# Kernel tuning notes

Measured on AMD Instinct MI355X. Metric: run time of the kernel, lower is better.

Reference implementation:

```python
import jax, jax.numpy as jnp
import numpy as np

ARITY = 4  # matches init_kwargs; params.shape[1] == 2**ARITY


def _high_order_act(X, params):
    # X: [B, G*arity], params: [G, 2**arity, O]
    B = X.shape[0]
    G, _, O = params.shape
    a = ARITY
    A = X.reshape(B, G, a)
    # sort ascending along the arity dim (torch.sort returns values + indices)
    A_ind = jnp.argsort(A, axis=2)                      # [B, G, a] int32
    A_sort = jnp.take_along_axis(A, A_ind, axis=2)      # [B, G, a]
    # barycentric-style coefficients: smallest value, then successive diffs
    coef = jnp.concatenate(
        [A_sort[:, :, :1], A_sort[:, :, 1:] - A_sort[:, :, :-1]], axis=2
    )                                                   # [B, G, a]
    # bit-power index: reverse cumsum of 2**A_ind -> suffix sums of bit masks
    pow2 = jnp.left_shift(jnp.int32(1), A_ind.astype(jnp.int32))  # [B, G, a]
    idx = jnp.cumsum(pow2[:, :, ::-1], axis=2)[:, :, ::-1]        # [B, G, a], in [1, 2**a - 1]
    # gather per-group table rows: params[g, idx[b,g,k], :]
    g_idx = jnp.arange(G)[None, :, None]                # [1, G, 1]
    gathered = params[g_idx, idx]                       # [B, G, a, O]
    # einsum 'jikl,ijk->ijl' in torch (j=G, i=B) == 'bgao,bga->bgo' here
    out = jnp.einsum('bgao,bga->bgo', gathered, coef)   # [B, G, O]
    return out.reshape(B, G * O)


def setup_inputs() -> dict:
    key = jax.random.key(0)
    kx, kp = jax.random.split(key)
    B, G, a, O = 8192, 256, ARITY, 16
    X = jax.random.normal(kx, (B, G * a), dtype=jnp.float32)
    params = jax.random.normal(kp, (G, 2 ** a, O), dtype=jnp.float32)
    return {"X": X, "params": params}


def reference(X, params):
    return _high_order_act(X, params)
```

## Files before the change

### kernel.cpp

```cpp
#include <hip/hip_runtime.h>


typedef float f32x4 __attribute__((ext_vector_type(4)));

#define NT 512
#define TG 16
#define ROWS 64
#define RPW 8
#define TSTRIDE 260

__global__ __launch_bounds__(NT, 4) void hoa_kernel(
    const float* __restrict__ X, const float* __restrict__ P,
    float* __restrict__ out, int B, int G)
{
    __shared__ float lds[TG * TSTRIDE];

    const int tid = threadIdx.x;
    const int g0 = blockIdx.x * TG;
    const int b0 = blockIdx.y * ROWS;

#pragma unroll
    for (int i = 0; i < 2; ++i) {
        int idx = tid + i * NT;
        int table = idx >> 6;
        int within = idx & 63;
        f32x4 v = *reinterpret_cast<const f32x4*>(
            P + (size_t)(g0 + table) * 256 + within * 4);
        *reinterpret_cast<f32x4*>(&lds[table * TSTRIDE + within * 4]) = v;
    }
    __syncthreads();

    const int c  = tid & 3;
    const int gg = (tid >> 2) & 15;
    const int wv = tid >> 6;
    const int g  = g0 + gg;
    const int brow = b0 + wv * RPW;

    const float* tab = &lds[gg * TSTRIDE + c * 4];
    const float* xp  = X   + (size_t)brow * (G * 4)  + g * 4;
    float*       op  = out + (size_t)brow * (G * 16) + g * 16 + c * 4;
    const size_t xstride = (size_t)G * 4;
    const size_t ostride = (size_t)G * 16;

    f32x4 xs[RPW];
#pragma unroll
    for (int r = 0; r < RPW; ++r) {
        if (brow + r < B)
            xs[r] = *reinterpret_cast<const f32x4*>(xp + r * xstride);
    }

#pragma unroll
    for (int r = 0; r < RPW; ++r) {
        if (brow + r >= B) continue;
        float v0 = xs[r].x, v1 = xs[r].y, v2 = xs[r].z, v3 = xs[r].w;
        int i0 = 0, i1 = 1, i2 = 2, i3 = 3;

#define CSWAP(va, vb, ia, ib)                         \
        {                                             \
            bool sw_ = (va) > (vb);                   \
            float lo_ = sw_ ? (vb) : (va);            \
            float hi_ = sw_ ? (va) : (vb);            \
            int il_ = sw_ ? (ib) : (ia);              \
            int ih_ = sw_ ? (ia) : (ib);              \
            (va) = lo_; (vb) = hi_; (ia) = il_; (ib) = ih_; \
        }
        CSWAP(v0, v1, i0, i1);
        CSWAP(v2, v3, i2, i3);
        CSWAP(v0, v2, i0, i2);
        CSWAP(v1, v3, i1, i3);
        CSWAP(v1, v2, i1, i2);
#undef CSWAP

        float c0 = v0, c1 = v1 - v0, c2 = v2 - v1, c3 = v3 - v2;
        int idx0 = 15;
        int idx1 = 15 ^ (1 << i0);
        int idx2 = idx1 ^ (1 << i1);
        int idx3 = 1 << i3;

        f32x4 A  = *reinterpret_cast<const f32x4*>(tab + idx0 * 16);
        f32x4 Bv = *reinterpret_cast<const f32x4*>(tab + idx1 * 16);
        f32x4 C  = *reinterpret_cast<const f32x4*>(tab + idx2 * 16);
        f32x4 D  = *reinterpret_cast<const f32x4*>(tab + idx3 * 16);

        f32x4 o;
        o.x = fmaf(c3, D.x, fmaf(c2, C.x, fmaf(c1, Bv.x, c0 * A.x)));
        o.y = fmaf(c3, D.y, fmaf(c2, C.y, fmaf(c1, Bv.y, c0 * A.y)));
        o.z = fmaf(c3, D.z, fmaf(c2, C.z, fmaf(c1, Bv.z, c0 * A.z)));
        o.w = fmaf(c3, D.w, fmaf(c2, C.w, fmaf(c1, Bv.w, c0 * A.w)));

        *reinterpret_cast<f32x4*>(op + r * ostride) = o;
    }
}

extern "C" void kernel_launch(void* const* d_in, const int* in_sizes, int n_in,
                              void* d_out, int out_size, void* d_ws, size_t ws_size,
                              hipStream_t stream) {
    const float* X = (const float*)d_in[0];
    const float* P = (const float*)d_in[1];
    float* out = (float*)d_out;

    int G = in_sizes[1] / 256;
    int B = in_sizes[0] / (G * 4);

    dim3 grid(G / TG, (B + ROWS - 1) / ROWS);
    hipLaunchKernelGGL(hoa_kernel, grid, dim3(NT), 0, stream, X, P, out, B, G);
}
```

Baseline: 157.7 us.

## Assign one thread per group for all outputs with swizzled LDS tables

Work is remapped so each thread owns one whole group and computes all 16 outputs for 4 rows. Before, four threads shared each group and each repeated the same sort. Blocks grow to 1024 threads covering 64 groups, and the LDS tables are XOR-swizzled to reduce bank conflicts on the now divergent per-thread table reads. The aim is to remove the redundant sorting and index math. In exchange, each store instruction now has lanes 64 bytes apart instead of contiguous, LDS per block rises, and the grid shrinks to fewer, larger blocks, which may hurt occupancy and coalescing.

```diff
diff --git a/kernel.cpp b/kernel.cpp
--- a/kernel.cpp
+++ b/kernel.cpp
@@ -3,11 +3,54 @@
 
 typedef float f32x4 __attribute__((ext_vector_type(4)));
 
-#define NT 512
-#define TG 16
+#define NT 1024
+#define TG 64
 #define ROWS 64
-#define RPW 8
+#define WPB 16
 #define TSTRIDE 260
+
+__device__ __forceinline__ void row_compute_store(
+    f32x4 x, const float* tab, int key, float* obase)
+{
+    float v0 = x.x, v1 = x.y, v2 = x.z, v3 = x.w;
+    int i0 = 0, i1 = 1, i2 = 2, i3 = 3;
+
+#define CSWAP(va, vb, ia, ib)                         \
+    {                                                 \
+        bool sw_ = (va) > (vb);                       \
+        float lo_ = sw_ ? (vb) : (va);                \
+        float hi_ = sw_ ? (va) : (vb);                \
+        int il_ = sw_ ? (ib) : (ia);                  \
+        int ih_ = sw_ ? (ia) : (ib);                  \
+        (va) = lo_; (vb) = hi_; (ia) = il_; (ib) = ih_; \
+    }
+    CSWAP(v0, v1, i0, i1);
+    CSWAP(v2, v3, i2, i3);
+    CSWAP(v0, v2, i0, i2);
+    CSWAP(v1, v3, i1, i3);
+    CSWAP(v1, v2, i1, i2);
+#undef CSWAP
+
+    float c0 = v0, c1 = v1 - v0, c2 = v2 - v1, c3 = v3 - v2;
+    int idx0 = 15;
+    int idx1 = 15 ^ (1 << i0);
+    int idx2 = idx1 ^ (1 << i1);
+    int idx3 = 1 << i3;
+
+#pragma unroll
+    for (int k = 0; k < 4; ++k) {
+        f32x4 A  = *reinterpret_cast<const f32x4*>(tab + 4 * ((idx0 * 4 + k) ^ key));
+        f32x4 Bv = *reinterpret_cast<const f32x4*>(tab + 4 * ((idx1 * 4 + k) ^ key));
+        f32x4 C  = *reinterpret_cast<const f32x4*>(tab + 4 * ((idx2 * 4 + k) ^ key));
+        f32x4 D  = *reinterpret_cast<const f32x4*>(tab + 4 * ((idx3 * 4 + k) ^ key));
+        f32x4 o;
+        o.x = fmaf(c3, D.x, fmaf(c2, C.x, fmaf(c1, Bv.x, c0 * A.x)));
+        o.y = fmaf(c3, D.y, fmaf(c2, C.y, fmaf(c1, Bv.y, c0 * A.y)));
+        o.z = fmaf(c3, D.z, fmaf(c2, C.z, fmaf(c1, Bv.z, c0 * A.z)));
+        o.w = fmaf(c3, D.w, fmaf(c2, C.w, fmaf(c1, Bv.w, c0 * A.w)));
+        *reinterpret_cast<f32x4*>(obase + k * 4) = o;
+    }
+}
 
 __global__ __launch_bounds__(NT, 4) void hoa_kernel(
     const float* __restrict__ X, const float* __restrict__ P,
@@ -20,76 +63,36 @@
     const int b0 = blockIdx.y * ROWS;
 
 #pragma unroll
-    for (int i = 0; i < 2; ++i) {
+    for (int i = 0; i < (TG * 64) / NT; ++i) {
         int idx = tid + i * NT;
-        int table = idx >> 6;
-        int within = idx & 63;
+        int t = idx >> 6;
+        int w = idx & 63;
         f32x4 v = *reinterpret_cast<const f32x4*>(
-            P + (size_t)(g0 + table) * 256 + within * 4);
-        *reinterpret_cast<f32x4*>(&lds[table * TSTRIDE + within * 4]) = v;
+            P + (size_t)(g0 + t) * 256 + w * 4);
+        int ws = w ^ ((t >> 3) & 7);
+        *reinterpret_cast<f32x4*>(&lds[t * TSTRIDE + ws * 4]) = v;
     }
     __syncthreads();
 
-    const int c  = tid & 3;
-    const int gg = (tid >> 2) & 15;
+    const int gg = tid & 63;
     const int wv = tid >> 6;
     const int g  = g0 + gg;
-    const int brow = b0 + wv * RPW;
+    const float* tab = &lds[gg * TSTRIDE];
+    const int key = (gg >> 3) & 7;
 
-    const float* tab = &lds[gg * TSTRIDE + c * 4];
-    const float* xp  = X   + (size_t)brow * (G * 4)  + g * 4;
-    float*       op  = out + (size_t)brow * (G * 16) + g * 16 + c * 4;
-    const size_t xstride = (size_t)G * 4;
-    const size_t ostride = (size_t)G * 16;
+    const int r0 = b0 + wv;
+    const int r1 = r0 + WPB, r2 = r1 + WPB, r3 = r2 + WPB;
 
-    f32x4 xs[RPW];
-#pragma unroll
-    for (int r = 0; r < RPW; ++r) {
-        if (brow + r < B)
-            xs[r] = *reinterpret_cast<const f32x4*>(xp + r * xstride);
-    }
+    f32x4 x0, x1, x2, x3;
+    if (r0 < B) x0 = *reinterpret_cast<const f32x4*>(X + (size_t)r0 * (G * 4) + g * 4);
+    if (r1 < B) x1 = *reinterpret_cast<const f32x4*>(X + (size_t)r1 * (G * 4) + g * 4);
+    if (r2 < B) x2 = *reinterpret_cast<const f32x4*>(X + (size_t)r2 * (G * 4) + g * 4);
+    if (r3 < B) x3 = *reinterpret_cast<const f32x4*>(X + (size_t)r3 * (G * 4) + g * 4);
 
-#pragma unroll
-    for (int r = 0; r < RPW; ++r) {
-        if (brow + r >= B) continue;
-        float v0 = xs[r].x, v1 = xs[r].y, v2 = xs[r].z, v3 = xs[r].w;
-        int i0 = 0, i1 = 1, i2 = 2, i3 = 3;
-
-#define CSWAP(va, vb, ia, ib)                         \
-        {                                             \
-            bool sw_ = (va) > (vb);                   \
-            float lo_ = sw_ ? (vb) : (va);            \
-            float hi_ = sw_ ? (va) : (vb);            \
-            int il_ = sw_ ? (ib) : (ia);              \
-            int ih_ = sw_ ? (ia) : (ib);              \
-            (va) = lo_; (vb) = hi_; (ia) = il_; (ib) = ih_; \
-        }
-        CSWAP(v0, v1, i0, i1);
-        CSWAP(v2, v3, i2, i3);
-        CSWAP(v0, v2, i0, i2);
-        CSWAP(v1, v3, i1, i3);
-        CSWAP(v1, v2, i1, i2);
-#undef CSWAP
-
-        float c0 = v0, c1 = v1 - v0, c2 = v2 - v1, c3 = v3 - v2;
-        int idx0 = 15;
-        int idx1 = 15 ^ (1 << i0);
-        int idx2 = idx1 ^ (1 << i1);
-        int idx3 = 1 << i3;
-
-        f32x4 A  = *reinterpret_cast<const f32x4*>(tab + idx0 * 16);
-        f32x4 Bv = *reinterpret_cast<const f32x4*>(tab + idx1 * 16);
-        f32x4 C  = *reinterpret_cast<const f32x4*>(tab + idx2 * 16);
-        f32x4 D  = *reinterpret_cast<const f32x4*>(tab + idx3 * 16);
-
-        f32x4 o;
-        o.x = fmaf(c3, D.x, fmaf(c2, C.x, fmaf(c1, Bv.x, c0 * A.x)));
-        o.y = fmaf(c3, D.y, fmaf(c2, C.y, fmaf(c1, Bv.y, c0 * A.y)));
-        o.z = fmaf(c3, D.z, fmaf(c2, C.z, fmaf(c1, Bv.z, c0 * A.z)));
-        o.w = fmaf(c3, D.w, fmaf(c2, C.w, fmaf(c1, Bv.w, c0 * A.w)));
-
-        *reinterpret_cast<f32x4*>(op + r * ostride) = o;
-    }
+    if (r0 < B) row_compute_store(x0, tab, key, out + (size_t)r0 * (G * 16) + (size_t)g * 16);
+    if (r1 < B) row_compute_store(x1, tab, key, out + (size_t)r1 * (G * 16) + (size_t)g * 16);
+    if (r2 < B) row_compute_store(x2, tab, key, out + (size_t)r2 * (G * 16) + (size_t)g * 16);
+    if (r3 < B) row_compute_store(x3, tab, key, out + (size_t)r3 * (G * 16) + (size_t)g * 16);
 }
 
 extern "C" void kernel_launch(void* const* d_in, const int* in_sizes, int n_in,
```

Result: slower. 176.0 us (+11.6%).
